# Optimization experiments

Hardware: AMD Instinct MI355X
Metric: run time of the kernel (lower is better)

## Reference

```python
import jax, jax.numpy as jnp
import numpy as np

BS, N, IN_NF, H, EH, OUT_NF, L = 16, 128, 64, 256, 128, 64, 4
C = 1.0


def _lin(k, fan_in, fan_out):
    s = 1.0 / np.sqrt(fan_in)
    return jax.random.uniform(k, (fan_in, fan_out), minval=-s, maxval=s, dtype=jnp.float32)


def setup_inputs() -> dict:
    key = jax.random.key(0)
    ks = jax.random.split(key, 8)
    # fully-connected directed edges (i != j), offset per graph in the batch
    r = np.repeat(np.arange(N), N)
    c = np.tile(np.arange(N), N)
    m = r != c
    r, c = r[m], c[m]  # [N*(N-1)]
    off = (np.arange(BS) * N)[:, None]
    rows = jnp.asarray((r[None, :] + off).reshape(-1), dtype=jnp.int32)  # [BS*N*(N-1)]
    cols = jnp.asarray((c[None, :] + off).reshape(-1), dtype=jnp.int32)

    def stack(kb, fan_in, fan_out):
        return jnp.stack([_lin(jax.random.fold_in(kb, l), fan_in, fan_out) for l in range(L)])

    return {
        "h": jax.random.normal(ks[0], (BS, N, IN_NF), dtype=jnp.float32),
        "rows": rows,
        "cols": cols,
        "w_in": _lin(ks[1], IN_NF, H), "b_in": jnp.zeros((H,), jnp.float32),
        "w_out": _lin(ks[2], H, OUT_NF), "b_out": jnp.zeros((OUT_NF,), jnp.float32),
        "we1": stack(ks[3], 2 * H, EH), "be1": jnp.zeros((L, EH), jnp.float32),
        "we2": stack(ks[4], EH, EH), "be2": jnp.zeros((L, EH), jnp.float32),
        "wn1": stack(ks[5], H + EH, H), "bn1": jnp.zeros((L, H), jnp.float32),
        "wn2": stack(ks[6], H, H), "bn2": jnp.zeros((L, H), jnp.float32),
    }


def reference(h, rows, cols, w_in, b_in, w_out, b_out,
              we1, be1, we2, be2, wn1, bn1, wn2, bn2):
    bs, n, _ = h.shape
    ntot = bs * n
    x = h.reshape(ntot, -1) @ w_in + b_in  # embedding_in -> [ntot, H]
    for l in range(L):  # stacked GCL layers (small fixed count)
        # edge model: gather endpoints, MLP on concatenated pair features
        m = jnp.concatenate([x[rows], x[cols]], axis=-1)        # [E, 2H]
        m = jax.nn.silu(m @ we1[l] + be1[l])                     # [E, EH]
        m = jax.nn.silu(m @ we2[l] + be2[l])                     # [E, EH]
        # node model: scatter-sum messages back to receiver nodes
        agg = jax.ops.segment_sum(m, rows, num_segments=ntot) * C  # [ntot, EH]
        u = jnp.concatenate([x, agg], axis=-1)                   # [ntot, H+EH]
        u = jax.nn.silu(u @ wn1[l] + bn1[l])
        u = u @ wn2[l] + bn2[l]
        x = x + u  # residual
    return x @ w_out + b_out  # embedding_out -> [ntot, OUT_NF]
```

## Files before the change

kernel.cpp:

```cpp
#include <hip/hip_runtime.h>

#define NTOT 2048
#define INF 64
#define HD 256
#define EHD 128
#define ONF 64
#define NL 4

typedef __attribute__((ext_vector_type(8))) short bf16x8;
typedef __attribute__((ext_vector_type(4))) float f32x4;

__device__ __forceinline__ float silu_f(float v) {
    return v * __builtin_amdgcn_rcpf(1.0f + __expf(-v));
}

__device__ __forceinline__ unsigned short f2bf_rn(float f) {
    unsigned u = __float_as_uint(f);
    u += 0x7FFFu + ((u >> 16) & 1u);
    return (unsigned short)(u >> 16);
}
__device__ __forceinline__ void split_rn(float v, unsigned short& h, unsigned short& l) {
    h = f2bf_rn(v);
    l = f2bf_rn(v - __uint_as_float((unsigned)h << 16));
}
__device__ __forceinline__ void split_tr(float v, unsigned& uh, unsigned& ul) {
    unsigned u = __float_as_uint(v);
    uh = u & 0xffff0000u;
    ul = __float_as_uint(v - __uint_as_float(uh)) & 0xffff0000u;
}
__device__ __forceinline__ float bfraw2f(unsigned short s) {
    return __uint_as_float((unsigned)s << 16);
}

__global__ __launch_bounds__(256) void k_prep(
        const float* __restrict__ w_in, const float* __restrict__ we1,
        const float* __restrict__ wn1, const float* __restrict__ wn2,
        const float* __restrict__ w_out, const float* __restrict__ we2,
        short* __restrict__ hwin, short* __restrict__ lwin,
        short* __restrict__ hwe1, short* __restrict__ lwe1,
        short* __restrict__ hwn1, short* __restrict__ lwn1,
        short* __restrict__ hwn2, short* __restrict__ lwn2,
        short* __restrict__ hwout, short* __restrict__ lwout,
        short* __restrict__ hwe2) {
    const int gid = blockIdx.x * 256 + threadIdx.x;
    const float* src; short* hd; short* ld;
    int sl, dst, KS, N, mode;
    if (gid < 2048)        { sl = gid;                dst = gid;           src = w_in;                                  hd = hwin;  ld = lwin;  KS = 2;  N = 256; mode = 0; }
    else if (gid < 34816)  { int g = gid - 2048;      sl = g & 8191;  dst = g; src = we1 + (size_t)(g >> 13) * 512 * 128;   hd = hwe1;  ld = lwe1;  KS = 8;  N = 256; mode = 1; }
    else if (gid < 83968)  { int g = gid - 34816;     sl = g % 12288; dst = g; src = wn1 + (size_t)(g / 12288) * 384 * 256; hd = hwn1;  ld = lwn1;  KS = 12; N = 256; mode = 0; }
    else if (gid < 116736) { int g = gid - 83968;     sl = g & 8191;  dst = g; src = wn2 + (size_t)(g >> 13) * 256 * 256;   hd = hwn2;  ld = lwn2;  KS = 8;  N = 256; mode = 0; }
    else if (gid < 118784) { int g = gid - 116736;    sl = g;         dst = g; src = w_out;                                 hd = hwout; ld = lwout; KS = 8;  N = 64;  mode = 0; }
    else if (gid < 126976) { int g = gid - 118784;    sl = g & 2047;  dst = g; src = we2 + (size_t)(g >> 11) * 128 * 128;   hd = hwe2;  ld = 0;     KS = 4;  N = 128; mode = 0; }
    else return;
    const int lane = sl & 63;
    const int t2 = sl >> 6;
    const int ks = t2 % KS;
    const int nt = t2 / KS;
    const int n = nt * 16 + (lane & 15);
    const int k0 = ks * 32 + ((lane >> 4) << 3);
    short h8[8], l8[8];
#pragma unroll
    for (int i = 0; i < 8; ++i) {
        int k = k0 + i;
        float f;
        if (mode == 1) f = (n < 128) ? src[(size_t)k * 128 + n] : src[(size_t)(256 + k) * 128 + (n - 128)];
        else           f = src[(size_t)k * N + n];
        unsigned short hh, ll;
        split_rn(f, hh, ll);
        h8[i] = (short)hh; l8[i] = (short)ll;
    }
#pragma unroll
    for (int i = 0; i < 8; ++i) hd[(size_t)dst * 8 + i] = h8[i];
    if (ld) {
#pragma unroll
        for (int i = 0; i < 8; ++i) ld[(size_t)dst * 8 + i] = l8[i];
    }
}

__global__ __launch_bounds__(1024, 4) void k_embed_ab(
        const float* __restrict__ h, const float* __restrict__ b_in,
        const float* __restrict__ be1,
        const short* __restrict__ hwin, const short* __restrict__ lwin,
        const short* __restrict__ hwe1, const short* __restrict__ lwe1,
        short* __restrict__ xs_hi, short* __restrict__ xs_lo,
        float* __restrict__ A, float* __restrict__ Bb) {
    __shared__ __align__(16) short hls[2][2][64][8];
    __shared__ __align__(16) short xls[2][8][64][8];
    const int t = threadIdx.x;
    const int mt = blockIdx.x;
    const int n0 = mt * 16;
    const int w = t >> 6, lane = t & 63;
    const int r0 = (lane >> 4) * 4;

    {
        const int m = t >> 6, k = t & 63;
        float v = h[(size_t)(n0 + m) * INF + k];
        unsigned uh, ul;
        split_tr(v, uh, ul);
        const int ks = k >> 5;
        const int lane2 = m + 16 * ((k & 31) >> 3);
        const int i0 = k & 7;
        hls[0][ks][lane2][i0] = (short)(uh >> 16);
        hls[1][ks][lane2][i0] = (short)(ul >> 16);
    }
    __syncthreads();
    f32x4 acc = {0.f, 0.f, 0.f, 0.f};
#pragma unroll
    for (int ks = 0; ks < 2; ++ks) {
        bf16x8 ah = *(const bf16x8*)&hls[0][ks][lane][0];
        bf16x8 al = *(const bf16x8*)&hls[1][ks][lane][0];
        bf16x8 bh = ((const bf16x8*)hwin)[(w * 2 + ks) * 64 + lane];
        bf16x8 bl = ((const bf16x8*)lwin)[(w * 2 + ks) * 64 + lane];
        acc = __builtin_amdgcn_mfma_f32_16x16x32_bf16(ah, bh, acc, 0, 0, 0);
        acc = __builtin_amdgcn_mfma_f32_16x16x32_bf16(al, bh, acc, 0, 0, 0);
        acc = __builtin_amdgcn_mfma_f32_16x16x32_bf16(ah, bl, acc, 0, 0, 0);
    }
    {
        int col = w * 16 + (lane & 15);
        float bias = b_in[col];
        int ks = col >> 5, l2b = 16 * ((col & 31) >> 3), i2 = col & 7;
#pragma unroll
        for (int reg = 0; reg < 4; ++reg) {
            float xv = acc[reg] + bias;
            unsigned uh, ul;
            split_tr(xv, uh, ul);
            xls[0][ks][r0 + reg + l2b][i2] = (short)(uh >> 16);
            xls[1][ks][r0 + reg + l2b][i2] = (short)(ul >> 16);
        }
    }
    __syncthreads();
    {
        int s = t;
        int plane = s >> 9, ks = (s >> 6) & 7, ln = s & 63;
        bf16x8 v = *(const bf16x8*)&xls[plane][ks][ln][0];
        bf16x8* dstp = (bf16x8*)(plane ? xs_lo : xs_hi);
        dstp[(size_t)(mt * 8 + ks) * 64 + ln] = v;
    }
    f32x4 acc1 = {0.f, 0.f, 0.f, 0.f};
#pragma unroll
    for (int ks = 0; ks < 8; ++ks) {
        bf16x8 ah = *(const bf16x8*)&xls[0][ks][lane][0];
        bf16x8 al = *(const bf16x8*)&xls[1][ks][lane][0];
        bf16x8 bh = ((const bf16x8*)hwe1)[(w * 8 + ks) * 64 + lane];
        bf16x8 bl = ((const bf16x8*)lwe1)[(w * 8 + ks) * 64 + lane];
        acc1 = __builtin_amdgcn_mfma_f32_16x16x32_bf16(ah, bh, acc1, 0, 0, 0);
        acc1 = __builtin_amdgcn_mfma_f32_16x16x32_bf16(al, bh, acc1, 0, 0, 0);
        acc1 = __builtin_amdgcn_mfma_f32_16x16x32_bf16(ah, bl, acc1, 0, 0, 0);
    }
    {
        int j = w * 16 + (lane & 15);
        float bias = (j < 128) ? be1[j] : 0.0f;
        float* dstp = (j < 128) ? A : Bb;
        int jj = j & 127;
#pragma unroll
        for (int reg = 0; reg < 4; ++reg) {
            int node = n0 + r0 + reg;
            dstp[(size_t)node * 128 + jj] = acc1[reg] + bias;
        }
    }
}

__global__ __launch_bounds__(512, 4) void k_edge_mfma(
        const float* __restrict__ A, const float* __restrict__ Bb,
        const short* __restrict__ hwe2,
        const float* __restrict__ be2, float* __restrict__ agg) {
    __shared__ __align__(16) short fr[4][2][4][64][8];
    __shared__ float red[2][4][2][16];
    const int n = blockIdx.x;
    const int b0 = n & ~127;
    const int r = n & 127;
    const int t = threadIdx.x;
    const int w = t >> 6, lane = t & 63;
    const int sh = w >> 2, jt = w & 3;

#pragma unroll
    for (int i = 0; i < 4; ++i) {
        const int E = i * 512 + t;
        const int c = E >> 4, ko = E & 15;
        const int ks = ko >> 2;
        const float4 bv0 = *(const float4*)&Bb[(size_t)(b0 + c) * EHD + ko * 8];
        const float4 bv1 = *(const float4*)&Bb[(size_t)(b0 + c) * EHD + ko * 8 + 4];
        const float4 av0 = *(const float4*)&A[(size_t)n * EHD + ko * 8];
        const float4 av1 = *(const float4*)&A[(size_t)n * EHD + ko * 8 + 4];
        float v[8] = {bv0.x + av0.x, bv0.y + av0.y, bv0.z + av0.z, bv0.w + av0.w,
                      bv1.x + av1.x, bv1.y + av1.y, bv1.z + av1.z, bv1.w + av1.w};
        unsigned short rb[8];
#pragma unroll
        for (int j = 0; j < 8; ++j) rb[j] = f2bf_rn(silu_f(v[j]));
        uint4 ph;
        ph.x = (unsigned)rb[0] | ((unsigned)rb[1] << 16);
        ph.y = (unsigned)rb[2] | ((unsigned)rb[3] << 16);
        ph.z = (unsigned)rb[4] | ((unsigned)rb[5] << 16);
        ph.w = (unsigned)rb[6] | ((unsigned)rb[7] << 16);
        const int lf = (c & 15) | ((ko & 3) << 4);
        *(uint4*)&fr[c >> 5][(c >> 4) & 1][ks][lf ^ (ks << 1)][0] = ph;
    }

    bf16x8 bh[2][4];
#pragma unroll
    for (int nti = 0; nti < 2; ++nti) {
        const int nt = jt * 2 + nti;
#pragma unroll
        for (int ks = 0; ks < 4; ++ks)
            bh[nti][ks] = ((const bf16x8*)hwe2)[(nt * 4 + ks) * 64 + lane];
    }
    float be2v[2];
#pragma unroll
    for (int nti = 0; nti < 2; ++nti)
        be2v[nti] = be2[(jt * 2 + nti) * 16 + (lane & 15)];

    __syncthreads();

    float colsum[2] = {0.0f, 0.0f};
#pragma unroll
    for (int chl = 0; chl < 2; ++chl) {
        const int ch = sh * 2 + chl;
#pragma unroll
        for (int mtl = 0; mtl < 2; ++mtl) {
            bf16x8 ah[4];
#pragma unroll
            for (int ks = 0; ks < 4; ++ks)
                ah[ks] = *(const bf16x8*)&fr[ch][mtl][ks][lane ^ (ks << 1)][0];
            const int cbase = ch * 32 + mtl * 16 + ((lane >> 4) << 2);
#pragma unroll
            for (int nti = 0; nti < 2; ++nti) {
                f32x4 a = {0.0f, 0.0f, 0.0f, 0.0f};
#pragma unroll
                for (int ks = 0; ks < 4; ++ks)
                    a = __builtin_amdgcn_mfma_f32_16x16x32_bf16(ah[ks], bh[nti][ks], a, 0, 0, 0);
#pragma unroll
                for (int reg = 0; reg < 4; ++reg) {
                    const int c = cbase + reg;
                    float s = silu_f(a[reg] + be2v[nti]);
                    colsum[nti] += (c != r) ? s : 0.0f;
                }
            }
        }
    }
#pragma unroll
    for (int nti = 0; nti < 2; ++nti) {
        float s = colsum[nti];
        s += __shfl_xor(s, 16);
        s += __shfl_xor(s, 32);
        if (lane < 16) red[sh][jt][nti][lane] = s;
    }
    __syncthreads();
    if (t < 128) {
        const int jtf = t >> 5, ntif = (t >> 4) & 1, j16 = t & 15;
        agg[(size_t)n * EHD + jtf * 32 + ntif * 16 + j16] =
            red[0][jtf][ntif][j16] + red[1][jtf][ntif][j16];
    }
}

__global__ __launch_bounds__(1024, 4) void k_node_ab(
        const float* __restrict__ agg,
        const float* __restrict__ bn1, const float* __restrict__ bn2,
        const float* __restrict__ be1, const float* __restrict__ b_out,
        const short* __restrict__ hwn1, const short* __restrict__ lwn1,
        const short* __restrict__ hwn2, const short* __restrict__ lwn2,
        const short* __restrict__ hwe1, const short* __restrict__ lwe1,
        const short* __restrict__ hwout, const short* __restrict__ lwout,
        short* __restrict__ xs_hi, short* __restrict__ xs_lo,
        float* __restrict__ A, float* __restrict__ Bb,
        float* __restrict__ outp, int last) {
    __shared__ __align__(16) short cat[2][12][64][8];
    __shared__ __align__(16) short u1[2][8][64][8];
    __shared__ __align__(16) short xn[2][8][64][8];
    const int t = threadIdx.x;
    const int mt = blockIdx.x;
    const int n0 = mt * 16;
    const int w = t >> 6, lane = t & 63;
    const int r0 = (lane >> 4) * 4;

    {
        int s = t;
        int plane = s >> 9, ks = (s >> 6) & 7, ln = s & 63;
        const bf16x8* srcp = (const bf16x8*)(plane ? xs_lo : xs_hi);
        bf16x8 v = srcp[(size_t)(mt * 8 + ks) * 64 + ln];
        *(bf16x8*)&cat[plane][ks][ln][0] = v;
    }
    {
        const int m = t >> 6;
        const int kq = t & 63;
        const int k0 = kq * 2;
        const float2 v2 = *(const float2*)&agg[(size_t)(n0 + m) * EHD + k0];
        unsigned uh0, ul0, uh1, ul1;
        split_tr(v2.x, uh0, ul0);
        split_tr(v2.y, uh1, ul1);
        const int ks = 8 + (k0 >> 5);
        const int lane2 = m + 16 * ((k0 & 31) >> 3);
        const int i0 = k0 & 7;
        *(unsigned*)&cat[0][ks][lane2][i0] = (uh0 >> 16) | uh1;
        *(unsigned*)&cat[1][ks][lane2][i0] = (ul0 >> 16) | ul1;
    }
    __syncthreads();
    f32x4 acc = {0.f, 0.f, 0.f, 0.f};
#pragma unroll
    for (int ks = 0; ks < 12; ++ks) {
        bf16x8 ah = *(const bf16x8*)&cat[0][ks][lane][0];
        bf16x8 al = *(const bf16x8*)&cat[1][ks][lane][0];
        bf16x8 bh = ((const bf16x8*)hwn1)[(w * 12 + ks) * 64 + lane];
        bf16x8 bl = ((const bf16x8*)lwn1)[(w * 12 + ks) * 64 + lane];
        acc = __builtin_amdgcn_mfma_f32_16x16x32_bf16(ah, bh, acc, 0, 0, 0);
        acc = __builtin_amdgcn_mfma_f32_16x16x32_bf16(al, bh, acc, 0, 0, 0);
        acc = __builtin_amdgcn_mfma_f32_16x16x32_bf16(ah, bl, acc, 0, 0, 0);
    }
    const int col = w * 16 + (lane & 15);
    const int ksu = col >> 5, l2b = 16 * ((col & 31) >> 3), i2 = col & 7;
    {
        float bias = bn1[col];
#pragma unroll
        for (int reg = 0; reg < 4; ++reg) {
            float uv = silu_f(acc[reg] + bias);
            unsigned uh, ul;
            split_tr(uv, uh, ul);
            u1[0][ksu][r0 + reg + l2b][i2] = (short)(uh >> 16);
            u1[1][ksu][r0 + reg + l2b][i2] = (short)(ul >> 16);
        }
    }
    __syncthreads();
    f32x4 acc2 = {0.f, 0.f, 0.f, 0.f};
#pragma unroll
    for (int ks = 0; ks < 8; ++ks) {
        bf16x8 ah = *(const bf16x8*)&u1[0][ks][lane][0];
        bf16x8 al = *(const bf16x8*)&u1[1][ks][lane][0];
        bf16x8 bh = ((const bf16x8*)hwn2)[(w * 8 + ks) * 64 + lane];
        bf16x8 bl = ((const bf16x8*)lwn2)[(w * 8 + ks) * 64 + lane];
        acc2 = __builtin_amdgcn_mfma_f32_16x16x32_bf16(ah, bh, acc2, 0, 0, 0);
        acc2 = __builtin_amdgcn_mfma_f32_16x16x32_bf16(al, bh, acc2, 0, 0, 0);
        acc2 = __builtin_amdgcn_mfma_f32_16x16x32_bf16(ah, bl, acc2, 0, 0, 0);
    }
    {
        float bias = bn2[col];
#pragma unroll
        for (int reg = 0; reg < 4; ++reg) {
            int lane2 = r0 + reg + l2b;
            float xold = bfraw2f((unsigned short)cat[0][ksu][lane2][i2])
                       + bfraw2f((unsigned short)cat[1][ksu][lane2][i2]);
            float xv = acc2[reg] + bias + xold;
            unsigned uh, ul;
            split_tr(xv, uh, ul);
            xn[0][ksu][lane2][i2] = (short)(uh >> 16);
            xn[1][ksu][lane2][i2] = (short)(ul >> 16);
        }
    }
    __syncthreads();
    if (!last) {
        {
            int s = t;
            int plane = s >> 9, ks = (s >> 6) & 7, ln = s & 63;
            bf16x8 v = *(const bf16x8*)&xn[plane][ks][ln][0];
            bf16x8* dstp = (bf16x8*)(plane ? xs_lo : xs_hi);
            dstp[(size_t)(mt * 8 + ks) * 64 + ln] = v;
        }
        f32x4 acc3 = {0.f, 0.f, 0.f, 0.f};
#pragma unroll
        for (int ks = 0; ks < 8; ++ks) {
            bf16x8 ah = *(const bf16x8*)&xn[0][ks][lane][0];
            bf16x8 al = *(const bf16x8*)&xn[1][ks][lane][0];
            bf16x8 bh = ((const bf16x8*)hwe1)[(w * 8 + ks) * 64 + lane];
            bf16x8 bl = ((const bf16x8*)lwe1)[(w * 8 + ks) * 64 + lane];
            acc3 = __builtin_amdgcn_mfma_f32_16x16x32_bf16(ah, bh, acc3, 0, 0, 0);
            acc3 = __builtin_amdgcn_mfma_f32_16x16x32_bf16(al, bh, acc3, 0, 0, 0);
            acc3 = __builtin_amdgcn_mfma_f32_16x16x32_bf16(ah, bl, acc3, 0, 0, 0);
        }
        {
            int j = col;
            float bias = (j < 128) ? be1[j] : 0.0f;
            float* dstp = (j < 128) ? A : Bb;
            int jj = j & 127;
#pragma unroll
            for (int reg = 0; reg < 4; ++reg) {
                int node = n0 + r0 + reg;
                dstp[(size_t)node * 128 + jj] = acc3[reg] + bias;
            }
        }
    } else if (w < 4) {
        f32x4 acco = {0.f, 0.f, 0.f, 0.f};
#pragma unroll
        for (int ks = 0; ks < 8; ++ks) {
            bf16x8 ah = *(const bf16x8*)&xn[0][ks][lane][0];
            bf16x8 al = *(const bf16x8*)&xn[1][ks][lane][0];
            bf16x8 bh = ((const bf16x8*)hwout)[(w * 8 + ks) * 64 + lane];
            bf16x8 bl = ((const bf16x8*)lwout)[(w * 8 + ks) * 64 + lane];
            acco = __builtin_amdgcn_mfma_f32_16x16x32_bf16(ah, bh, acco, 0, 0, 0);
            acco = __builtin_amdgcn_mfma_f32_16x16x32_bf16(al, bh, acco, 0, 0, 0);
            acco = __builtin_amdgcn_mfma_f32_16x16x32_bf16(ah, bl, acco, 0, 0, 0);
        }
        float bias = b_out[col];
#pragma unroll
        for (int reg = 0; reg < 4; ++reg) {
            outp[(size_t)(n0 + r0 + reg) * ONF + col] = acco[reg] + bias;
        }
    }
}

extern "C" void kernel_launch(void* const* d_in, const int* in_sizes, int n_in,
                              void* d_out, int out_size, void* d_ws, size_t ws_size,
                              hipStream_t stream) {
    const float* h     = (const float*)d_in[0];
    const float* w_in  = (const float*)d_in[3];
    const float* b_in  = (const float*)d_in[4];
    const float* w_out = (const float*)d_in[5];
    const float* b_out = (const float*)d_in[6];
    const float* we1   = (const float*)d_in[7];
    const float* be1   = (const float*)d_in[8];
    const float* we2   = (const float*)d_in[9];
    const float* be2   = (const float*)d_in[10];
    const float* wn1   = (const float*)d_in[11];
    const float* bn1   = (const float*)d_in[12];
    const float* wn2   = (const float*)d_in[13];
    const float* bn2   = (const float*)d_in[14];

    float* A    = (float*)d_ws;
    float* Bb   = A + 262144;
    float* agg  = Bb + 262144;
    short* xs_hi = (short*)(agg + 262144);
    short* xs_lo = xs_hi + 524288;
    short* hwin  = xs_lo + 524288;
    short* lwin  = hwin + 16384;
    short* hwe1  = lwin + 16384;
    short* lwe1  = hwe1 + 262144;
    short* hwn1  = lwe1 + 262144;
    short* lwn1  = hwn1 + 393216;
    short* hwn2  = lwn1 + 393216;
    short* lwn2  = hwn2 + 262144;
    short* hwout = lwn2 + 262144;
    short* lwout = hwout + 16384;
    short* hwe2  = lwout + 16384;
    float* outp  = (float*)d_out;

    k_prep<<<496, 256, 0, stream>>>(w_in, we1, wn1, wn2, w_out, we2,
        hwin, lwin, hwe1, lwe1, hwn1, lwn1, hwn2, lwn2, hwout, lwout, hwe2);
    k_embed_ab<<<128, 1024, 0, stream>>>(h, b_in, be1, hwin, lwin, hwe1, lwe1,
        xs_hi, xs_lo, A, Bb);
    for (int l = 0; l < NL; ++l) {
        const int last = (l == NL - 1);
        const int lp = last ? 0 : (l + 1);
        k_edge_mfma<<<NTOT, 512, 0, stream>>>(A, Bb,
            hwe2 + (size_t)l * 2048 * 8,
            be2 + l * EHD, agg);
        k_node_ab<<<128, 1024, 0, stream>>>(agg,
            bn1 + l * HD, bn2 + l * HD, be1 + lp * EHD, b_out,
            hwn1 + (size_t)l * 12288 * 8, lwn1 + (size_t)l * 12288 * 8,
            hwn2 + (size_t)l * 8192 * 8, lwn2 + (size_t)l * 8192 * 8,
            hwe1 + (size_t)lp * 8192 * 8, lwe1 + (size_t)lp * 8192 * 8,
            hwout, lwout, xs_hi, xs_lo, A, Bb, outp, last);
    }
}
```

Measured before the change: 170.2 us.

## Fuse all stages into one persistent cooperative kernel with grid syncs

Replaces the prep, embed, per-layer edge and node kernels with a single cooperative persistent kernel. Grid-wide syncs separate the stages, and each stage's work is distributed over blocks with grid-stride loops. Node and embed work moves from 1024-thread blocks to 512-thread blocks, with each wave computing two output tiles. This removes the per-launch overhead of about ten kernel launches. In exchange it adds grid-sync costs, and occupancy is capped by the 56KB shared memory buffer and the cooperative launch limits.

```diff
diff --git a/kernel.cpp b/kernel.cpp
--- a/kernel.cpp
+++ b/kernel.cpp
@@ -1,4 +1,7 @@
 #include <hip/hip_runtime.h>
+#include <hip/hip_cooperative_groups.h>
+
+namespace cg = cooperative_groups;
 
 #define NTOT 2048
 #define INF 64
@@ -13,7 +16,6 @@
 __device__ __forceinline__ float silu_f(float v) {
     return v * __builtin_amdgcn_rcpf(1.0f + __expf(-v));
 }
-
 __device__ __forceinline__ unsigned short f2bf_rn(float f) {
     unsigned u = __float_as_uint(f);
     u += 0x7FFFu + ((u >> 16) & 1u);
@@ -32,366 +34,388 @@
     return __uint_as_float((unsigned)s << 16);
 }
 
-__global__ __launch_bounds__(256) void k_prep(
-        const float* __restrict__ w_in, const float* __restrict__ we1,
-        const float* __restrict__ wn1, const float* __restrict__ wn2,
-        const float* __restrict__ w_out, const float* __restrict__ we2,
-        short* __restrict__ hwin, short* __restrict__ lwin,
-        short* __restrict__ hwe1, short* __restrict__ lwe1,
-        short* __restrict__ hwn1, short* __restrict__ lwn1,
-        short* __restrict__ hwn2, short* __restrict__ lwn2,
-        short* __restrict__ hwout, short* __restrict__ lwout,
-        short* __restrict__ hwe2) {
-    const int gid = blockIdx.x * 256 + threadIdx.x;
-    const float* src; short* hd; short* ld;
-    int sl, dst, KS, N, mode;
-    if (gid < 2048)        { sl = gid;                dst = gid;           src = w_in;                                  hd = hwin;  ld = lwin;  KS = 2;  N = 256; mode = 0; }
-    else if (gid < 34816)  { int g = gid - 2048;      sl = g & 8191;  dst = g; src = we1 + (size_t)(g >> 13) * 512 * 128;   hd = hwe1;  ld = lwe1;  KS = 8;  N = 256; mode = 1; }
-    else if (gid < 83968)  { int g = gid - 34816;     sl = g % 12288; dst = g; src = wn1 + (size_t)(g / 12288) * 384 * 256; hd = hwn1;  ld = lwn1;  KS = 12; N = 256; mode = 0; }
-    else if (gid < 116736) { int g = gid - 83968;     sl = g & 8191;  dst = g; src = wn2 + (size_t)(g >> 13) * 256 * 256;   hd = hwn2;  ld = lwn2;  KS = 8;  N = 256; mode = 0; }
-    else if (gid < 118784) { int g = gid - 116736;    sl = g;         dst = g; src = w_out;                                 hd = hwout; ld = lwout; KS = 8;  N = 64;  mode = 0; }
-    else if (gid < 126976) { int g = gid - 118784;    sl = g & 2047;  dst = g; src = we2 + (size_t)(g >> 11) * 128 * 128;   hd = hwe2;  ld = 0;     KS = 4;  N = 128; mode = 0; }
-    else return;
-    const int lane = sl & 63;
-    const int t2 = sl >> 6;
-    const int ks = t2 % KS;
-    const int nt = t2 / KS;
-    const int n = nt * 16 + (lane & 15);
-    const int k0 = ks * 32 + ((lane >> 4) << 3);
-    short h8[8], l8[8];
-#pragma unroll
-    for (int i = 0; i < 8; ++i) {
-        int k = k0 + i;
-        float f;
-        if (mode == 1) f = (n < 128) ? src[(size_t)k * 128 + n] : src[(size_t)(256 + k) * 128 + (n - 128)];
-        else           f = src[(size_t)k * N + n];
-        unsigned short hh, ll;
-        split_rn(f, hh, ll);
-        h8[i] = (short)hh; l8[i] = (short)ll;
-    }
-#pragma unroll
-    for (int i = 0; i < 8; ++i) hd[(size_t)dst * 8 + i] = h8[i];
-    if (ld) {
-#pragma unroll
-        for (int i = 0; i < 8; ++i) ld[(size_t)dst * 8 + i] = l8[i];
-    }
-}
-
-__global__ __launch_bounds__(1024, 4) void k_embed_ab(
-        const float* __restrict__ h, const float* __restrict__ b_in,
-        const float* __restrict__ be1,
-        const short* __restrict__ hwin, const short* __restrict__ lwin,
-        const short* __restrict__ hwe1, const short* __restrict__ lwe1,
-        short* __restrict__ xs_hi, short* __restrict__ xs_lo,
-        float* __restrict__ A, float* __restrict__ Bb) {
-    __shared__ __align__(16) short hls[2][2][64][8];
-    __shared__ __align__(16) short xls[2][8][64][8];
+#define MFMA(a, b, c) __builtin_amdgcn_mfma_f32_16x16x32_bf16(a, b, c, 0, 0, 0)
+
+__global__ __launch_bounds__(512, 4) void k_mega(
+        const float* __restrict__ h, const float* __restrict__ w_in,
+        const float* __restrict__ b_in, const float* __restrict__ w_out,
+        const float* __restrict__ b_out, const float* __restrict__ we1,
+        const float* __restrict__ be1, const float* __restrict__ we2,
+        const float* __restrict__ be2, const float* __restrict__ wn1,
+        const float* __restrict__ bn1, const float* __restrict__ wn2,
+        const float* __restrict__ bn2, float* __restrict__ ws,
+        float* __restrict__ outp) {
+    cg::grid_group gg = cg::this_grid();
+    __shared__ __align__(16) char smem[57344];
+    const int bid = blockIdx.x;
+    const int nb = gridDim.x;
     const int t = threadIdx.x;
-    const int mt = blockIdx.x;
-    const int n0 = mt * 16;
     const int w = t >> 6, lane = t & 63;
     const int r0 = (lane >> 4) * 4;
 
-    {
-        const int m = t >> 6, k = t & 63;
-        float v = h[(size_t)(n0 + m) * INF + k];
-        unsigned uh, ul;
-        split_tr(v, uh, ul);
-        const int ks = k >> 5;
-        const int lane2 = m + 16 * ((k & 31) >> 3);
-        const int i0 = k & 7;
-        hls[0][ks][lane2][i0] = (short)(uh >> 16);
-        hls[1][ks][lane2][i0] = (short)(ul >> 16);
+    float* A     = ws;
+    float* Bb    = A + 262144;
+    float* agg   = Bb + 262144;
+    short* xs_hi = (short*)(agg + 262144);
+    short* xs_lo = xs_hi + 524288;
+    short* hwin  = xs_lo + 524288;
+    short* lwin  = hwin + 16384;
+    short* hwe1  = lwin + 16384;
+    short* lwe1  = hwe1 + 262144;
+    short* hwn1  = lwe1 + 262144;
+    short* lwn1  = hwn1 + 393216;
+    short* hwn2  = lwn1 + 393216;
+    short* lwn2  = hwn2 + 262144;
+    short* hwout = lwn2 + 262144;
+    short* lwout = hwout + 16384;
+    short* hwe2  = lwout + 16384;
+
+    for (int gid = bid * 512 + t; gid < 126976; gid += nb * 512) {
+        const float* src; short* hd; short* ld;
+        int sl, dst, KS, N, mode;
+        if (gid < 2048)        { sl = gid;             dst = gid; src = w_in;                                  hd = hwin;  ld = lwin;  KS = 2;  N = 256; mode = 0; }
+        else if (gid < 34816)  { int g = gid - 2048;   sl = g & 8191;  dst = g; src = we1 + (size_t)(g >> 13) * 512 * 128;   hd = hwe1;  ld = lwe1;  KS = 8;  N = 256; mode = 1; }
+        else if (gid < 83968)  { int g = gid - 34816;  sl = g % 12288; dst = g; src = wn1 + (size_t)(g / 12288) * 384 * 256; hd = hwn1;  ld = lwn1;  KS = 12; N = 256; mode = 0; }
+        else if (gid < 116736) { int g = gid - 83968;  sl = g & 8191;  dst = g; src = wn2 + (size_t)(g >> 13) * 256 * 256;   hd = hwn2;  ld = lwn2;  KS = 8;  N = 256; mode = 0; }
+        else if (gid < 118784) { int g = gid - 116736; sl = g;         dst = g; src = w_out;                                 hd = hwout; ld = lwout; KS = 8;  N = 64;  mode = 0; }
+        else                   { int g = gid - 118784; sl = g & 2047;  dst = g; src = we2 + (size_t)(g >> 11) * 128 * 128;   hd = hwe2;  ld = 0;     KS = 4;  N = 128; mode = 0; }
+        const int lanep = sl & 63;
+        const int t2 = sl >> 6;
+        const int ks = t2 % KS;
+        const int nt = t2 / KS;
+        const int n = nt * 16 + (lanep & 15);
+        const int k0 = ks * 32 + ((lanep >> 4) << 3);
+        short h8[8], l8[8];
+#pragma unroll
+        for (int i = 0; i < 8; ++i) {
+            int k = k0 + i;
+            float f;
+            if (mode == 1) f = (n < 128) ? src[(size_t)k * 128 + n] : src[(size_t)(256 + k) * 128 + (n - 128)];
+            else           f = src[(size_t)k * N + n];
+            unsigned short hh, ll;
+            split_rn(f, hh, ll);
+            h8[i] = (short)hh; l8[i] = (short)ll;
+        }
+#pragma unroll
+        for (int i = 0; i < 8; ++i) hd[(size_t)dst * 8 + i] = h8[i];
+        if (ld) {
+#pragma unroll
+            for (int i = 0; i < 8; ++i) ld[(size_t)dst * 8 + i] = l8[i];
+        }
     }
-    __syncthreads();
-    f32x4 acc = {0.f, 0.f, 0.f, 0.f};
-#pragma unroll
-    for (int ks = 0; ks < 2; ++ks) {
-        bf16x8 ah = *(const bf16x8*)&hls[0][ks][lane][0];
-        bf16x8 al = *(const bf16x8*)&hls[1][ks][lane][0];
-        bf16x8 bh = ((const bf16x8*)hwin)[(w * 2 + ks) * 64 + lane];
-        bf16x8 bl = ((const bf16x8*)lwin)[(w * 2 + ks) * 64 + lane];
-        acc = __builtin_amdgcn_mfma_f32_16x16x32_bf16(ah, bh, acc, 0, 0, 0);
-        acc = __builtin_amdgcn_mfma_f32_16x16x32_bf16(al, bh, acc, 0, 0, 0);
-        acc = __builtin_amdgcn_mfma_f32_16x16x32_bf16(ah, bl, acc, 0, 0, 0);
-    }
-    {
-        int col = w * 16 + (lane & 15);
-        float bias = b_in[col];
-        int ks = col >> 5, l2b = 16 * ((col & 31) >> 3), i2 = col & 7;
-#pragma unroll
-        for (int reg = 0; reg < 4; ++reg) {
-            float xv = acc[reg] + bias;
+    gg.sync();
+
+    for (int mt = bid; mt < 128; mt += nb) {
+        short (*hls)[2][64][8] = (short(*)[2][64][8])smem;
+        short (*xls)[8][64][8] = (short(*)[8][64][8])(smem + 4096);
+        const int n0 = mt * 16;
+#pragma unroll
+        for (int rep = 0; rep < 2; ++rep) {
+            int s = rep * 512 + t;
+            int m = s >> 6, k = s & 63;
+            float v = h[(size_t)(n0 + m) * INF + k];
             unsigned uh, ul;
-            split_tr(xv, uh, ul);
-            xls[0][ks][r0 + reg + l2b][i2] = (short)(uh >> 16);
-            xls[1][ks][r0 + reg + l2b][i2] = (short)(ul >> 16);
-        }
-    }
-    __syncthreads();
-    {
-        int s = t;
-        int plane = s >> 9, ks = (s >> 6) & 7, ln = s & 63;
-        bf16x8 v = *(const bf16x8*)&xls[plane][ks][ln][0];
-        bf16x8* dstp = (bf16x8*)(plane ? xs_lo : xs_hi);
-        dstp[(size_t)(mt * 8 + ks) * 64 + ln] = v;
-    }
-    f32x4 acc1 = {0.f, 0.f, 0.f, 0.f};
-#pragma unroll
-    for (int ks = 0; ks < 8; ++ks) {
-        bf16x8 ah = *(const bf16x8*)&xls[0][ks][lane][0];
-        bf16x8 al = *(const bf16x8*)&xls[1][ks][lane][0];
-        bf16x8 bh = ((const bf16x8*)hwe1)[(w * 8 + ks) * 64 + lane];
-        bf16x8 bl = ((const bf16x8*)lwe1)[(w * 8 + ks) * 64 + lane];
-        acc1 = __builtin_amdgcn_mfma_f32_16x16x32_bf16(ah, bh, acc1, 0, 0, 0);
-        acc1 = __builtin_amdgcn_mfma_f32_16x16x32_bf16(al, bh, acc1, 0, 0, 0);
-        acc1 = __builtin_amdgcn_mfma_f32_16x16x32_bf16(ah, bl, acc1, 0, 0, 0);
-    }
-    {
-        int j = w * 16 + (lane & 15);
-        float bias = (j < 128) ? be1[j] : 0.0f;
-        float* dstp = (j < 128) ? A : Bb;
-        int jj = j & 127;
-#pragma unroll
-        for (int reg = 0; reg < 4; ++reg) {
-            int node = n0 + r0 + reg;
-            dstp[(size_t)node * 128 + jj] = acc1[reg] + bias;
-        }
-    }
-}
-
-__global__ __launch_bounds__(512, 4) void k_edge_mfma(
-        const float* __restrict__ A, const float* __restrict__ Bb,
-        const short* __restrict__ hwe2,
-        const float* __restrict__ be2, float* __restrict__ agg) {
-    __shared__ __align__(16) short fr[4][2][4][64][8];
-    __shared__ float red[2][4][2][16];
-    const int n = blockIdx.x;
-    const int b0 = n & ~127;
-    const int r = n & 127;
-    const int t = threadIdx.x;
-    const int w = t >> 6, lane = t & 63;
-    const int sh = w >> 2, jt = w & 3;
-
-#pragma unroll
-    for (int i = 0; i < 4; ++i) {
-        const int E = i * 512 + t;
-        const int c = E >> 4, ko = E & 15;
-        const int ks = ko >> 2;
-        const float4 bv0 = *(const float4*)&Bb[(size_t)(b0 + c) * EHD + ko * 8];
-        const float4 bv1 = *(const float4*)&Bb[(size_t)(b0 + c) * EHD + ko * 8 + 4];
-        const float4 av0 = *(const float4*)&A[(size_t)n * EHD + ko * 8];
-        const float4 av1 = *(const float4*)&A[(size_t)n * EHD + ko * 8 + 4];
-        float v[8] = {bv0.x + av0.x, bv0.y + av0.y, bv0.z + av0.z, bv0.w + av0.w,
-                      bv1.x + av1.x, bv1.y + av1.y, bv1.z + av1.z, bv1.w + av1.w};
-        unsigned short rb[8];
-#pragma unroll
-        for (int j = 0; j < 8; ++j) rb[j] = f2bf_rn(silu_f(v[j]));
-        uint4 ph;
-        ph.x = (unsigned)rb[0] | ((unsigned)rb[1] << 16);
-        ph.y = (unsigned)rb[2] | ((unsigned)rb[3] << 16);
-        ph.z = (unsigned)rb[4] | ((unsigned)rb[5] << 16);
-        ph.w = (unsigned)rb[6] | ((unsigned)rb[7] << 16);
-        const int lf = (c & 15) | ((ko & 3) << 4);
-        *(uint4*)&fr[c >> 5][(c >> 4) & 1][ks][lf ^ (ks << 1)][0] = ph;
-    }
-
-    bf16x8 bh[2][4];
-#pragma unroll
-    for (int nti = 0; nti < 2; ++nti) {
-        const int nt = jt * 2 + nti;
-#pragma unroll
-        for (int ks = 0; ks < 4; ++ks)
-            bh[nti][ks] = ((const bf16x8*)hwe2)[(nt * 4 + ks) * 64 + lane];
-    }
-    float be2v[2];
-#pragma unroll
-    for (int nti = 0; nti < 2; ++nti)
-        be2v[nti] = be2[(jt * 2 + nti) * 16 + (lane & 15)];
-
-    __syncthreads();
-
-    float colsum[2] = {0.0f, 0.0f};
-#pragma unroll
-    for (int chl = 0; chl < 2; ++chl) {
-        const int ch = sh * 2 + chl;
-#pragma unroll
-        for (int mtl = 0; mtl < 2; ++mtl) {
-            bf16x8 ah[4];
-#pragma unroll
-            for (int ks = 0; ks < 4; ++ks)
-                ah[ks] = *(const bf16x8*)&fr[ch][mtl][ks][lane ^ (ks << 1)][0];
-            const int cbase = ch * 32 + mtl * 16 + ((lane >> 4) << 2);
-#pragma unroll
-            for (int nti = 0; nti < 2; ++nti) {
-                f32x4 a = {0.0f, 0.0f, 0.0f, 0.0f};
-#pragma unroll
-                for (int ks = 0; ks < 4; ++ks)
-                    a = __builtin_amdgcn_mfma_f32_16x16x32_bf16(ah[ks], bh[nti][ks], a, 0, 0, 0);
-#pragma unroll
-                for (int reg = 0; reg < 4; ++reg) {
-                    const int c = cbase + reg;
-                    float s = silu_f(a[reg] + be2v[nti]);
-                    colsum[nti] += (c != r) ? s : 0.0f;
-                }
-            }
-        }
-    }
-#pragma unroll
-    for (int nti = 0; nti < 2; ++nti) {
-        float s = colsum[nti];
-        s += __shfl_xor(s, 16);
-        s += __shfl_xor(s, 32);
-        if (lane < 16) red[sh][jt][nti][lane] = s;
-    }
-    __syncthreads();
-    if (t < 128) {
-        const int jtf = t >> 5, ntif = (t >> 4) & 1, j16 = t & 15;
-        agg[(size_t)n * EHD + jtf * 32 + ntif * 16 + j16] =
-            red[0][jtf][ntif][j16] + red[1][jtf][ntif][j16];
-    }
-}
-
-__global__ __launch_bounds__(1024, 4) void k_node_ab(
-        const float* __restrict__ agg,
-        const float* __restrict__ bn1, const float* __restrict__ bn2,
-        const float* __restrict__ be1, const float* __restrict__ b_out,
-        const short* __restrict__ hwn1, const short* __restrict__ lwn1,
-        const short* __restrict__ hwn2, const short* __restrict__ lwn2,
-        const short* __restrict__ hwe1, const short* __restrict__ lwe1,
-        const short* __restrict__ hwout, const short* __restrict__ lwout,
-        short* __restrict__ xs_hi, short* __restrict__ xs_lo,
-        float* __restrict__ A, float* __restrict__ Bb,
-        float* __restrict__ outp, int last) {
-    __shared__ __align__(16) short cat[2][12][64][8];
-    __shared__ __align__(16) short u1[2][8][64][8];
-    __shared__ __align__(16) short xn[2][8][64][8];
-    const int t = threadIdx.x;
-    const int mt = blockIdx.x;
-    const int n0 = mt * 16;
-    const int w = t >> 6, lane = t & 63;
-    const int r0 = (lane >> 4) * 4;
-
-    {
-        int s = t;
-        int plane = s >> 9, ks = (s >> 6) & 7, ln = s & 63;
-        const bf16x8* srcp = (const bf16x8*)(plane ? xs_lo : xs_hi);
-        bf16x8 v = srcp[(size_t)(mt * 8 + ks) * 64 + ln];
-        *(bf16x8*)&cat[plane][ks][ln][0] = v;
-    }
-    {
-        const int m = t >> 6;
-        const int kq = t & 63;
-        const int k0 = kq * 2;
-        const float2 v2 = *(const float2*)&agg[(size_t)(n0 + m) * EHD + k0];
-        unsigned uh0, ul0, uh1, ul1;
-        split_tr(v2.x, uh0, ul0);
-        split_tr(v2.y, uh1, ul1);
-        const int ks = 8 + (k0 >> 5);
-        const int lane2 = m + 16 * ((k0 & 31) >> 3);
-        const int i0 = k0 & 7;
-        *(unsigned*)&cat[0][ks][lane2][i0] = (uh0 >> 16) | uh1;
-        *(unsigned*)&cat[1][ks][lane2][i0] = (ul0 >> 16) | ul1;
-    }
-    __syncthreads();
-    f32x4 acc = {0.f, 0.f, 0.f, 0.f};
-#pragma unroll
-    for (int ks = 0; ks < 12; ++ks) {
-        bf16x8 ah = *(const bf16x8*)&cat[0][ks][lane][0];
-        bf16x8 al = *(const bf16x8*)&cat[1][ks][lane][0];
-        bf16x8 bh = ((const bf16x8*)hwn1)[(w * 12 + ks) * 64 + lane];
-        bf16x8 bl = ((const bf16x8*)lwn1)[(w * 12 + ks) * 64 + lane];
-        acc = __builtin_amdgcn_mfma_f32_16x16x32_bf16(ah, bh, acc, 0, 0, 0);
-        acc = __builtin_amdgcn_mfma_f32_16x16x32_bf16(al, bh, acc, 0, 0, 0);
-        acc = __builtin_amdgcn_mfma_f32_16x16x32_bf16(ah, bl, acc, 0, 0, 0);
-    }
-    const int col = w * 16 + (lane & 15);
-    const int ksu = col >> 5, l2b = 16 * ((col & 31) >> 3), i2 = col & 7;
-    {
-        float bias = bn1[col];
-#pragma unroll
-        for (int reg = 0; reg < 4; ++reg) {
-            float uv = silu_f(acc[reg] + bias);
-            unsigned uh, ul;
-            split_tr(uv, uh, ul);
-            u1[0][ksu][r0 + reg + l2b][i2] = (short)(uh >> 16);
-            u1[1][ksu][r0 + reg + l2b][i2] = (short)(ul >> 16);
-        }
-    }
-    __syncthreads();
-    f32x4 acc2 = {0.f, 0.f, 0.f, 0.f};
-#pragma unroll
-    for (int ks = 0; ks < 8; ++ks) {
-        bf16x8 ah = *(const bf16x8*)&u1[0][ks][lane][0];
-        bf16x8 al = *(const bf16x8*)&u1[1][ks][lane][0];
-        bf16x8 bh = ((const bf16x8*)hwn2)[(w * 8 + ks) * 64 + lane];
-        bf16x8 bl = ((const bf16x8*)lwn2)[(w * 8 + ks) * 64 + lane];
-        acc2 = __builtin_amdgcn_mfma_f32_16x16x32_bf16(ah, bh, acc2, 0, 0, 0);
-        acc2 = __builtin_amdgcn_mfma_f32_16x16x32_bf16(al, bh, acc2, 0, 0, 0);
-        acc2 = __builtin_amdgcn_mfma_f32_16x16x32_bf16(ah, bl, acc2, 0, 0, 0);
-    }
-    {
-        float bias = bn2[col];
-#pragma unroll
-        for (int reg = 0; reg < 4; ++reg) {
-            int lane2 = r0 + reg + l2b;
-            float xold = bfraw2f((unsigned short)cat[0][ksu][lane2][i2])
-                       + bfraw2f((unsigned short)cat[1][ksu][lane2][i2]);
-            float xv = acc2[reg] + bias + xold;
-            unsigned uh, ul;
-            split_tr(xv, uh, ul);
-            xn[0][ksu][lane2][i2] = (short)(uh >> 16);
-            xn[1][ksu][lane2][i2] = (short)(ul >> 16);
-        }
-    }
-    __syncthreads();
-    if (!last) {
-        {
-            int s = t;
+            split_tr(v, uh, ul);
+            int ks = k >> 5, lane2 = m + 16 * ((k & 31) >> 3), i0 = k & 7;
+            hls[0][ks][lane2][i0] = (short)(uh >> 16);
+            hls[1][ks][lane2][i0] = (short)(ul >> 16);
+        }
+        __syncthreads();
+        f32x4 acc[2];
+#pragma unroll
+        for (int nti2 = 0; nti2 < 2; ++nti2) {
+            const int nt = w * 2 + nti2;
+            f32x4 a = {0.f, 0.f, 0.f, 0.f};
+#pragma unroll
+            for (int ks = 0; ks < 2; ++ks) {
+                bf16x8 ah = *(const bf16x8*)&hls[0][ks][lane][0];
+                bf16x8 al = *(const bf16x8*)&hls[1][ks][lane][0];
+                bf16x8 bh = ((const bf16x8*)hwin)[(nt * 2 + ks) * 64 + lane];
+                bf16x8 bl = ((const bf16x8*)lwin)[(nt * 2 + ks) * 64 + lane];
+                a = MFMA(ah, bh, a); a = MFMA(al, bh, a); a = MFMA(ah, bl, a);
+            }
+            acc[nti2] = a;
+        }
+#pragma unroll
+        for (int nti2 = 0; nti2 < 2; ++nti2) {
+            int col = (w * 2 + nti2) * 16 + (lane & 15);
+            float bias = b_in[col];
+            int ks = col >> 5, l2b = 16 * ((col & 31) >> 3), i2 = col & 7;
+#pragma unroll
+            for (int reg = 0; reg < 4; ++reg) {
+                float xv = acc[nti2][reg] + bias;
+                unsigned uh, ul;
+                split_tr(xv, uh, ul);
+                xls[0][ks][r0 + reg + l2b][i2] = (short)(uh >> 16);
+                xls[1][ks][r0 + reg + l2b][i2] = (short)(ul >> 16);
+            }
+        }
+        __syncthreads();
+#pragma unroll
+        for (int rep = 0; rep < 2; ++rep) {
+            int s = rep * 512 + t;
             int plane = s >> 9, ks = (s >> 6) & 7, ln = s & 63;
-            bf16x8 v = *(const bf16x8*)&xn[plane][ks][ln][0];
+            bf16x8 v = *(const bf16x8*)&xls[plane][ks][ln][0];
             bf16x8* dstp = (bf16x8*)(plane ? xs_lo : xs_hi);
             dstp[(size_t)(mt * 8 + ks) * 64 + ln] = v;
         }
-        f32x4 acc3 = {0.f, 0.f, 0.f, 0.f};
-#pragma unroll
-        for (int ks = 0; ks < 8; ++ks) {
-            bf16x8 ah = *(const bf16x8*)&xn[0][ks][lane][0];
-            bf16x8 al = *(const bf16x8*)&xn[1][ks][lane][0];
-            bf16x8 bh = ((const bf16x8*)hwe1)[(w * 8 + ks) * 64 + lane];
-            bf16x8 bl = ((const bf16x8*)lwe1)[(w * 8 + ks) * 64 + lane];
-            acc3 = __builtin_amdgcn_mfma_f32_16x16x32_bf16(ah, bh, acc3, 0, 0, 0);
-            acc3 = __builtin_amdgcn_mfma_f32_16x16x32_bf16(al, bh, acc3, 0, 0, 0);
-            acc3 = __builtin_amdgcn_mfma_f32_16x16x32_bf16(ah, bl, acc3, 0, 0, 0);
-        }
-        {
-            int j = col;
+#pragma unroll
+        for (int nti2 = 0; nti2 < 2; ++nti2) {
+            const int nt = w * 2 + nti2;
+            f32x4 a = {0.f, 0.f, 0.f, 0.f};
+#pragma unroll
+            for (int ks = 0; ks < 8; ++ks) {
+                bf16x8 ah = *(const bf16x8*)&xls[0][ks][lane][0];
+                bf16x8 al = *(const bf16x8*)&xls[1][ks][lane][0];
+                bf16x8 bh = ((const bf16x8*)hwe1)[(nt * 8 + ks) * 64 + lane];
+                bf16x8 bl = ((const bf16x8*)lwe1)[(nt * 8 + ks) * 64 + lane];
+                a = MFMA(ah, bh, a); a = MFMA(al, bh, a); a = MFMA(ah, bl, a);
+            }
+            int j = nt * 16 + (lane & 15);
             float bias = (j < 128) ? be1[j] : 0.0f;
             float* dstp = (j < 128) ? A : Bb;
             int jj = j & 127;
 #pragma unroll
-            for (int reg = 0; reg < 4; ++reg) {
-                int node = n0 + r0 + reg;
-                dstp[(size_t)node * 128 + jj] = acc3[reg] + bias;
-            }
-        }
-    } else if (w < 4) {
-        f32x4 acco = {0.f, 0.f, 0.f, 0.f};
-#pragma unroll
-        for (int ks = 0; ks < 8; ++ks) {
-            bf16x8 ah = *(const bf16x8*)&xn[0][ks][lane][0];
-            bf16x8 al = *(const bf16x8*)&xn[1][ks][lane][0];
-            bf16x8 bh = ((const bf16x8*)hwout)[(w * 8 + ks) * 64 + lane];
-            bf16x8 bl = ((const bf16x8*)lwout)[(w * 8 + ks) * 64 + lane];
-            acco = __builtin_amdgcn_mfma_f32_16x16x32_bf16(ah, bh, acco, 0, 0, 0);
-            acco = __builtin_amdgcn_mfma_f32_16x16x32_bf16(al, bh, acco, 0, 0, 0);
-            acco = __builtin_amdgcn_mfma_f32_16x16x32_bf16(ah, bl, acco, 0, 0, 0);
-        }
-        float bias = b_out[col];
-#pragma unroll
-        for (int reg = 0; reg < 4; ++reg) {
-            outp[(size_t)(n0 + r0 + reg) * ONF + col] = acco[reg] + bias;
-        }
+            for (int reg = 0; reg < 4; ++reg)
+                dstp[(size_t)(n0 + r0 + reg) * 128 + jj] = a[reg] + bias;
+        }
+        __syncthreads();
+    }
+    gg.sync();
+
+    for (int l = 0; l < NL; ++l) {
+        {
+            short (*fr)[2][4][64][8] = (short(*)[2][4][64][8])smem;
+            float (*red)[4][2][16]   = (float(*)[4][2][16])(smem + 32768);
+            const short* hwe2l = hwe2 + (size_t)l * 2048 * 8;
+            const int sh = w >> 2, jt = w & 3;
+            const int ko = t & 15;
+            const int ksw = ko >> 2;
+            const int lfbase = (ko & 3) << 4;
+            const int mtl_s = (t >> 8) & 1;
+            const int c15 = (t >> 4) & 15;
+            bf16x8 bh2[2][4];
+#pragma unroll
+            for (int nti = 0; nti < 2; ++nti)
+#pragma unroll
+                for (int ks = 0; ks < 4; ++ks)
+                    bh2[nti][ks] = ((const bf16x8*)hwe2l)[((jt * 2 + nti) * 4 + ks) * 64 + lane];
+            float be2v[2];
+#pragma unroll
+            for (int nti = 0; nti < 2; ++nti)
+                be2v[nti] = be2[l * EHD + (jt * 2 + nti) * 16 + (lane & 15)];
+
+            for (int n = bid; n < NTOT; n += nb) {
+                const int b0 = n & ~127, r = n & 127;
+                const float4 av0 = *(const float4*)&A[(size_t)n * EHD + ko * 8];
+                const float4 av1 = *(const float4*)&A[(size_t)n * EHD + ko * 8 + 4];
+#pragma unroll
+                for (int i = 0; i < 4; ++i) {
+                    const int c = i * 32 + (t >> 4);
+                    const float4 bv0 = *(const float4*)&Bb[(size_t)(b0 + c) * EHD + ko * 8];
+                    const float4 bv1 = *(const float4*)&Bb[(size_t)(b0 + c) * EHD + ko * 8 + 4];
+                    float v[8] = {bv0.x + av0.x, bv0.y + av0.y, bv0.z + av0.z, bv0.w + av0.w,
+                                  bv1.x + av1.x, bv1.y + av1.y, bv1.z + av1.z, bv1.w + av1.w};
+                    unsigned short rb[8];
+#pragma unroll
+                    for (int j = 0; j < 8; ++j) rb[j] = f2bf_rn(silu_f(v[j]));
+                    uint4 ph;
+                    ph.x = (unsigned)rb[0] | ((unsigned)rb[1] << 16);
+                    ph.y = (unsigned)rb[2] | ((unsigned)rb[3] << 16);
+                    ph.z = (unsigned)rb[4] | ((unsigned)rb[5] << 16);
+                    ph.w = (unsigned)rb[6] | ((unsigned)rb[7] << 16);
+                    const int lf = c15 | lfbase;
+                    *(uint4*)&fr[i][mtl_s][ksw][lf ^ (ksw << 1)][0] = ph;
+                }
+                __syncthreads();
+                float colsum[2] = {0.0f, 0.0f};
+#pragma unroll
+                for (int chl = 0; chl < 2; ++chl) {
+                    const int ch = sh * 2 + chl;
+#pragma unroll
+                    for (int mtl = 0; mtl < 2; ++mtl) {
+                        bf16x8 ah[4];
+#pragma unroll
+                        for (int ks = 0; ks < 4; ++ks)
+                            ah[ks] = *(const bf16x8*)&fr[ch][mtl][ks][lane ^ (ks << 1)][0];
+                        const int cbase = ch * 32 + mtl * 16 + ((lane >> 4) << 2);
+#pragma unroll
+                        for (int nti = 0; nti < 2; ++nti) {
+                            f32x4 a = {0.0f, 0.0f, 0.0f, 0.0f};
+#pragma unroll
+                            for (int ks = 0; ks < 4; ++ks)
+                                a = MFMA(ah[ks], bh2[nti][ks], a);
+#pragma unroll
+                            for (int reg = 0; reg < 4; ++reg) {
+                                const int c = cbase + reg;
+                                float s = silu_f(a[reg] + be2v[nti]);
+                                colsum[nti] += (c != r) ? s : 0.0f;
+                            }
+                        }
+                    }
+                }
+#pragma unroll
+                for (int nti = 0; nti < 2; ++nti) {
+                    float s = colsum[nti];
+                    s += __shfl_xor(s, 16);
+                    s += __shfl_xor(s, 32);
+                    if (lane < 16) red[sh][jt][nti][lane] = s;
+                }
+                __syncthreads();
+                if (t < 128) {
+                    const int jtf = t >> 5, ntif = (t >> 4) & 1, j16 = t & 15;
+                    agg[(size_t)n * EHD + jtf * 32 + ntif * 16 + j16] =
+                        red[0][jtf][ntif][j16] + red[1][jtf][ntif][j16];
+                }
+                __syncthreads();
+            }
+        }
+        gg.sync();
+
+        const int last = (l == NL - 1);
+        for (int mt = bid; mt < 128; mt += nb) {
+            short (*cat)[12][64][8] = (short(*)[12][64][8])smem;
+            short (*u1x)[8][64][8]  = (short(*)[8][64][8])(smem + 24576);
+            short (*xnx)[8][64][8]  = (short(*)[8][64][8])(smem + 40960);
+            const short* hwn1l = hwn1 + (size_t)l * 12288 * 8;
+            const short* lwn1l = lwn1 + (size_t)l * 12288 * 8;
+            const short* hwn2l = hwn2 + (size_t)l * 8192 * 8;
+            const short* lwn2l = lwn2 + (size_t)l * 8192 * 8;
+            const int lp = last ? 0 : (l + 1);
+            const short* hwe1n = hwe1 + (size_t)lp * 8192 * 8;
+            const short* lwe1n = lwe1 + (size_t)lp * 8192 * 8;
+            const int n0 = mt * 16;
+#pragma unroll
+            for (int rep = 0; rep < 2; ++rep) {
+                int s = rep * 512 + t;
+                int plane = s >> 9, ks = (s >> 6) & 7, ln = s & 63;
+                const bf16x8* srcp = (const bf16x8*)(plane ? xs_lo : xs_hi);
+                *(bf16x8*)&cat[plane][ks][ln][0] = srcp[(size_t)(mt * 8 + ks) * 64 + ln];
+            }
+            {
+                const int m = t >> 5, kq = t & 31, k0 = kq * 4;
+                const float4 v4 = *(const float4*)&agg[(size_t)(n0 + m) * EHD + k0];
+                unsigned uh0, ul0, uh1, ul1, uh2, ul2, uh3, ul3;
+                split_tr(v4.x, uh0, ul0); split_tr(v4.y, uh1, ul1);
+                split_tr(v4.z, uh2, ul2); split_tr(v4.w, uh3, ul3);
+                const int ks = 8 + (k0 >> 5);
+                const int lane2 = m + 16 * ((k0 & 31) >> 3);
+                const int i0 = k0 & 7;
+                *(uint2*)&cat[0][ks][lane2][i0] = make_uint2((uh0 >> 16) | uh1, (uh2 >> 16) | uh3);
+                *(uint2*)&cat[1][ks][lane2][i0] = make_uint2((ul0 >> 16) | ul1, (ul2 >> 16) | ul3);
+            }
+            __syncthreads();
+            f32x4 acc1[2];
+#pragma unroll
+            for (int nti2 = 0; nti2 < 2; ++nti2) {
+                const int nt = w * 2 + nti2;
+                f32x4 a = {0.f, 0.f, 0.f, 0.f};
+#pragma unroll
+                for (int ks = 0; ks < 12; ++ks) {
+                    bf16x8 ah = *(const bf16x8*)&cat[0][ks][lane][0];
+                    bf16x8 al = *(const bf16x8*)&cat[1][ks][lane][0];
+                    bf16x8 bh = ((const bf16x8*)hwn1l)[(nt * 12 + ks) * 64 + lane];
+                    bf16x8 bl = ((const bf16x8*)lwn1l)[(nt * 12 + ks) * 64 + lane];
+                    a = MFMA(ah, bh, a); a = MFMA(al, bh, a); a = MFMA(ah, bl, a);
+                }
+                acc1[nti2] = a;
+            }
+#pragma unroll
+            for (int nti2 = 0; nti2 < 2; ++nti2) {
+                const int col = (w * 2 + nti2) * 16 + (lane & 15);
+                const int ksu = col >> 5, l2b = 16 * ((col & 31) >> 3), i2 = col & 7;
+                float bias = bn1[l * HD + col];
+#pragma unroll
+                for (int reg = 0; reg < 4; ++reg) {
+                    float uv = silu_f(acc1[nti2][reg] + bias);
+                    unsigned uh, ul;
+                    split_tr(uv, uh, ul);
+                    u1x[0][ksu][r0 + reg + l2b][i2] = (short)(uh >> 16);
+                    u1x[1][ksu][r0 + reg + l2b][i2] = (short)(ul >> 16);
+                }
+            }
+            __syncthreads();
+            f32x4 acc2[2];
+#pragma unroll
+            for (int nti2 = 0; nti2 < 2; ++nti2) {
+                const int nt = w * 2 + nti2;
+                f32x4 a = {0.f, 0.f, 0.f, 0.f};
+#pragma unroll
+                for (int ks = 0; ks < 8; ++ks) {
+                    bf16x8 ah = *(const bf16x8*)&u1x[0][ks][lane][0];
+                    bf16x8 al = *(const bf16x8*)&u1x[1][ks][lane][0];
+                    bf16x8 bh = ((const bf16x8*)hwn2l)[(nt * 8 + ks) * 64 + lane];
+                    bf16x8 bl = ((const bf16x8*)lwn2l)[(nt * 8 + ks) * 64 + lane];
+                    a = MFMA(ah, bh, a); a = MFMA(al, bh, a); a = MFMA(ah, bl, a);
+                }
+                acc2[nti2] = a;
+            }
+#pragma unroll
+            for (int nti2 = 0; nti2 < 2; ++nti2) {
+                const int col = (w * 2 + nti2) * 16 + (lane & 15);
+                const int ksu = col >> 5, l2b = 16 * ((col & 31) >> 3), i2 = col & 7;
+                float bias = bn2[l * HD + col];
+#pragma unroll
+                for (int reg = 0; reg < 4; ++reg) {
+                    int lane2 = r0 + reg + l2b;
+                    float xold = bfraw2f((unsigned short)cat[0][ksu][lane2][i2])
+                               + bfraw2f((unsigned short)cat[1][ksu][lane2][i2]);
+                    float xv = acc2[nti2][reg] + bias + xold;
+                    unsigned uh, ul;
+                    split_tr(xv, uh, ul);
+                    xnx[0][ksu][lane2][i2] = (short)(uh >> 16);
+                    xnx[1][ksu][lane2][i2] = (short)(ul >> 16);
+                }
+            }
+            __syncthreads();
+            if (!last) {
+#pragma unroll
+                for (int rep = 0; rep < 2; ++rep) {
+                    int s = rep * 512 + t;
+                    int plane = s >> 9, ks = (s >> 6) & 7, ln = s & 63;
+                    bf16x8 v = *(const bf16x8*)&xnx[plane][ks][ln][0];
+                    bf16x8* dstp = (bf16x8*)(plane ? xs_lo : xs_hi);
+                    dstp[(size_t)(mt * 8 + ks) * 64 + ln] = v;
+                }
+#pragma unroll
+                for (int nti2 = 0; nti2 < 2; ++nti2) {
+                    const int nt = w * 2 + nti2;
+                    f32x4 a = {0.f, 0.f, 0.f, 0.f};
+#pragma unroll
+                    for (int ks = 0; ks < 8; ++ks) {
+                        bf16x8 ah = *(const bf16x8*)&xnx[0][ks][lane][0];
+                        bf16x8 al = *(const bf16x8*)&xnx[1][ks][lane][0];
+                        bf16x8 bh = ((const bf16x8*)hwe1n)[(nt * 8 + ks) * 64 + lane];
+                        bf16x8 bl = ((const bf16x8*)lwe1n)[(nt * 8 + ks) * 64 + lane];
+                        a = MFMA(ah, bh, a); a = MFMA(al, bh, a); a = MFMA(ah, bl, a);
+                    }
+                    int j = nt * 16 + (lane & 15);
+                    float bias = (j < 128) ? be1[lp * EHD + j] : 0.0f;
+                    float* dstp = (j < 128) ? A : Bb;
+                    int jj = j & 127;
+#pragma unroll
+                    for (int reg = 0; reg < 4; ++reg)
+                        dstp[(size_t)(n0 + r0 + reg) * 128 + jj] = a[reg] + bias;
+                }
+            } else if (w < 4) {
+                f32x4 a = {0.f, 0.f, 0.f, 0.f};
+#pragma unroll
+                for (int ks = 0; ks < 8; ++ks) {
+                    bf16x8 ah = *(const bf16x8*)&xnx[0][ks][lane][0];
+                    bf16x8 al = *(const bf16x8*)&xnx[1][ks][lane][0];
+                    bf16x8 bh = ((const bf16x8*)hwout)[(w * 8 + ks) * 64 + lane];
+                    bf16x8 bl = ((const bf16x8*)lwout)[(w * 8 + ks) * 64 + lane];
+                    a = MFMA(ah, bh, a); a = MFMA(al, bh, a); a = MFMA(ah, bl, a);
+                }
+                int col = w * 16 + (lane & 15);
+                float bias = b_out[col];
+#pragma unroll
+                for (int reg = 0; reg < 4; ++reg)
+                    outp[(size_t)(n0 + r0 + reg) * ONF + col] = a[reg] + bias;
+            }
+            __syncthreads();
+        }
+        if (!last) gg.sync();
     }
 }
 
@@ -411,40 +435,22 @@
     const float* bn1   = (const float*)d_in[12];
     const float* wn2   = (const float*)d_in[13];
     const float* bn2   = (const float*)d_in[14];
-
-    float* A    = (float*)d_ws;
-    float* Bb   = A + 262144;
-    float* agg  = Bb + 262144;
-    short* xs_hi = (short*)(agg + 262144);
-    short* xs_lo = xs_hi + 524288;
-    short* hwin  = xs_lo + 524288;
-    short* lwin  = hwin + 16384;
-    short* hwe1  = lwin + 16384;
-    short* lwe1  = hwe1 + 262144;
-    short* hwn1  = lwe1 + 262144;
-    short* lwn1  = hwn1 + 393216;
-    short* hwn2  = lwn1 + 393216;
-    short* lwn2  = hwn2 + 262144;
-    short* hwout = lwn2 + 262144;
-    short* lwout = hwout + 16384;
-    short* hwe2  = lwout + 16384;
-    float* outp  = (float*)d_out;
-
-    k_prep<<<496, 256, 0, stream>>>(w_in, we1, wn1, wn2, w_out, we2,
-        hwin, lwin, hwe1, lwe1, hwn1, lwn1, hwn2, lwn2, hwout, lwout, hwe2);
-    k_embed_ab<<<128, 1024, 0, stream>>>(h, b_in, be1, hwin, lwin, hwe1, lwe1,
-        xs_hi, xs_lo, A, Bb);
-    for (int l = 0; l < NL; ++l) {
-        const int last = (l == NL - 1);
-        const int lp = last ? 0 : (l + 1);
-        k_edge_mfma<<<NTOT, 512, 0, stream>>>(A, Bb,
-            hwe2 + (size_t)l * 2048 * 8,
-            be2 + l * EHD, agg);
-        k_node_ab<<<128, 1024, 0, stream>>>(agg,
-            bn1 + l * HD, bn2 + l * HD, be1 + lp * EHD, b_out,
-            hwn1 + (size_t)l * 12288 * 8, lwn1 + (size_t)l * 12288 * 8,
-            hwn2 + (size_t)l * 8192 * 8, lwn2 + (size_t)l * 8192 * 8,
-            hwe1 + (size_t)lp * 8192 * 8, lwe1 + (size_t)lp * 8192 * 8,
-            hwout, lwout, xs_hi, xs_lo, A, Bb, outp, last);
-    }
-}
+    float* ws   = (float*)d_ws;
+    float* outp = (float*)d_out;
+
+    int blocksPerCU = 0;
+    hipError_t qerr = hipOccupancyMaxActiveBlocksPerMultiprocessor(
+        &blocksPerCU, (const void*)k_mega, 512, 0);
+    if (qerr != hipSuccess || blocksPerCU < 1) blocksPerCU = 1;
+    int grid = blocksPerCU * 256;
+    if (grid > 512) grid = 512;
+
+    void* kargs[] = {
+        (void*)&h, (void*)&w_in, (void*)&b_in, (void*)&w_out, (void*)&b_out,
+        (void*)&we1, (void*)&be1, (void*)&we2, (void*)&be2,
+        (void*)&wn1, (void*)&bn1, (void*)&wn2, (void*)&bn2,
+        (void*)&ws, (void*)&outp
+    };
+    hipLaunchCooperativeKernel((const void*)k_mega, dim3(grid), dim3(512),
+                               kargs, 0, stream);
+}
```

Result: slower. 675.6 us (+296.9%).
